# Kernel optimization log

Measured on AMD Instinct MI355X. Metric: run time of the kernel, lower is better.

The kernel has to match this reference:

```python
import jax, jax.numpy as jnp
import numpy as np

SCALE = 2
GROUPS = 4


def setup_inputs() -> dict:
    key = jax.random.key(0)
    k1, k2 = jax.random.split(key)
    x = jax.random.normal(k1, (16, 64, 128, 128), dtype=jnp.float32)
    # offset conv: out_channels = 2*groups*scale^2 = 32, init std=0.001 as in normal_init
    w_off = jax.random.normal(k2, (32, 64), dtype=jnp.float32) * 0.001
    b_off = jnp.zeros((32,), dtype=jnp.float32)
    return {"x": x, "w_off": w_off, "b_off": b_off}


def _init_pos(dtype):
    # h = arange((-s+1)/2, (s-1)/2 + 1) / s ; for s=2 -> [-0.25, 0.25]
    h = (jnp.arange(SCALE, dtype=dtype) - (SCALE - 1) / 2.0) / SCALE
    # channel layout [2, groups, s*s] with p = i*s + j; d=0 -> h[j] (x), d=1 -> h[i] (y)
    hj = jnp.tile(h, SCALE)        # [s*s], value h[p % s]
    hi = jnp.repeat(h, SCALE)      # [s*s], value h[p // s]
    return jnp.stack([hj, hi])[:, None, :]  # [2, 1, s*s] broadcasts over groups


def _grid_sample_border(img, grid):
    # img: [N, C, H, W]; grid: [N, Ho, Wo, 2] in [-1,1], align_corners=False, border padding
    N, C, H, W = img.shape
    gx, gy = grid[..., 0], grid[..., 1]
    ix = jnp.clip(((gx + 1.0) * W - 1.0) * 0.5, 0.0, W - 1.0)
    iy = jnp.clip(((gy + 1.0) * H - 1.0) * 0.5, 0.0, H - 1.0)
    x0f = jnp.floor(ix); y0f = jnp.floor(iy)
    wx = ix - x0f; wy = iy - y0f
    x0 = jnp.clip(x0f.astype(jnp.int32), 0, W - 1)
    x1 = jnp.clip(x0 + 1, 0, W - 1)
    y0 = jnp.clip(y0f.astype(jnp.int32), 0, H - 1)
    y1 = jnp.clip(y0 + 1, 0, H - 1)

    gather = jax.vmap(lambda im, yy, xx: im[:, yy, xx])  # -> [N, C, Ho, Wo]
    v00 = gather(img, y0, x0)
    v01 = gather(img, y0, x1)
    v10 = gather(img, y1, x0)
    v11 = gather(img, y1, x1)
    wx = wx[:, None]; wy = wy[:, None]
    return (1 - wy) * ((1 - wx) * v00 + wx * v01) + wy * ((1 - wx) * v10 + wx * v11)


def reference(x, w_off, b_off):
    B, C, H, W = x.shape
    s, g = SCALE, GROUPS
    # 1x1 offset conv, lp style (no dyscope): offset = conv(x)*0.25 + init_pos
    off = jnp.einsum('bchw,oc->bohw', x, w_off) + b_off[None, :, None, None]
    off = off.reshape(B, 2, g, s * s, H, W) * 0.25 + _init_pos(x.dtype)[None, :, :, :, None, None]
    # pixel centers: x-coord = w+0.5, y-coord = h+0.5
    cx = (jnp.arange(W, dtype=x.dtype) + 0.5)[None, :]  # [1, W]
    cy = (jnp.arange(H, dtype=x.dtype) + 0.5)[:, None]  # [H, 1]
    base = jnp.stack([jnp.broadcast_to(cx, (H, W)), jnp.broadcast_to(cy, (H, W))])  # [2,H,W]
    norm = jnp.array([W, H], dtype=x.dtype).reshape(1, 2, 1, 1, 1, 1)
    coords = 2.0 * (base[None, :, None, None] + off) / norm - 1.0  # [B,2,g,s*s,H,W]
    # pixel_shuffle: output (h*s+i, w*s+j) takes sub-pixel p=i*s+j
    coords = coords.reshape(B, 2, g, s, s, H, W)
    coords = coords.transpose(0, 1, 2, 5, 3, 6, 4).reshape(B, 2, g, s * H, s * W)
    grid = coords.transpose(0, 2, 3, 4, 1).reshape(B * g, s * H, s * W, 2)  # [B*g,sH,sW,2]
    img = x.reshape(B * g, C // g, H, W)
    out = _grid_sample_border(img, grid)
    return out.reshape(B, C, s * H, s * W)
```

## Files before the change

kernel.cpp:

```cpp
#include <hip/hip_runtime.h>


__device__ __forceinline__ float bilerp(float a, float b, float c, float d,
                                        float wx, float wy) {
    const float top = fmaf(wx, b - a, a);
    const float bot = fmaf(wx, d - c, c);
    return fmaf(wy, bot - top, top);
}

__global__ __launch_bounds__(256, 4) void dysample_kernel(
    const float* __restrict__ x, const float* __restrict__ woff,
    const float* __restrict__ boff, float* __restrict__ out)
{
    const int bid = blockIdx.x;
    const int wg  = (bid & 7) * 128 + (bid >> 3);

    const int lane = threadIdx.x & 63;
    const int gr   = __builtin_amdgcn_readfirstlane(threadIdx.x >> 6);
    const int half = lane >> 5;
    const int c    = lane & 31;

    const int b  = wg >> 6;
    const int rp = wg & 63;
    const int h  = 2 * rp + half;

    const float* xb   = x + b * 1048576;
    const float* xrow = xb + h * 128 + 4 * c;

    float acc[8][4];
    #pragma unroll
    for (int j = 0; j < 8; ++j) {
        const float bv = boff[(j < 4) ? (gr * 4 + j) : (12 + gr * 4 + j)];
        #pragma unroll
        for (int p = 0; p < 4; ++p) acc[j][p] = bv;
    }

    #pragma unroll 8
    for (int ch = 0; ch < 64; ++ch) {
        const float4 v = *reinterpret_cast<const float4*>(xrow + ch * 16384);
        #pragma unroll
        for (int j = 0; j < 8; ++j) {
            const int o = (j < 4) ? (gr * 4 + j) : (12 + gr * 4 + j);
            const float wv = woff[o * 64 + ch];
            acc[j][0] = fmaf(v.x, wv, acc[j][0]);
            acc[j][1] = fmaf(v.y, wv, acc[j][1]);
            acc[j][2] = fmaf(v.z, wv, acc[j][2]);
            acc[j][3] = fmaf(v.w, wv, acc[j][3]);
        }
    }

    float wx[4][4], wy[4][4];
    const float fh = (float)h;
    #pragma unroll
    for (int p = 0; p < 4; ++p) {
        const float fwp = (float)(4 * c + p);
        wx[0][p] = fminf(fmaxf(fwp + 0.25f * acc[0][p] - 0.25f, 0.f), 127.f) - (fwp - 1.f);
        wx[1][p] = fminf(fmaxf(fwp + 0.25f * acc[1][p] + 0.25f, 0.f), 127.f) - fwp;
        wx[2][p] = fminf(fmaxf(fwp + 0.25f * acc[2][p] - 0.25f, 0.f), 127.f) - (fwp - 1.f);
        wx[3][p] = fminf(fmaxf(fwp + 0.25f * acc[3][p] + 0.25f, 0.f), 127.f) - fwp;
        wy[0][p] = fminf(fmaxf(fh  + 0.25f * acc[4][p] - 0.25f, 0.f), 127.f) - (fh - 1.f);
        wy[1][p] = fminf(fmaxf(fh  + 0.25f * acc[5][p] - 0.25f, 0.f), 127.f) - (fh - 1.f);
        wy[2][p] = fminf(fmaxf(fh  + 0.25f * acc[6][p] + 0.25f, 0.f), 127.f) - fh;
        wy[3][p] = fminf(fmaxf(fh  + 0.25f * acc[7][p] + 0.25f, 0.f), 127.f) - fh;
    }

    const int hOuter = half ? min(2 * rp + 2, 127) : max(2 * rp - 1, 0);
    const float* gpOuter = xb + gr * 262144 + hOuter * 128 + 4 * c;
    const float* gpMid   = xb + gr * 262144 + h * 128 + 4 * c;

    float* op = out + (size_t)(b * 64 + gr * 16) * 65536
              + (4 * rp + 2 * half) * 256 + 8 * c;

    #pragma unroll 2
    for (int cc = 0; cc < 16; ++cc) {
        const float4 vo = *reinterpret_cast<const float4*>(gpOuter + cc * 16384);
        const float4 vm = *reinterpret_cast<const float4*>(gpMid   + cc * 16384);
        float4 vs;
        vs.x = __shfl_xor(vm.x, 32); vs.y = __shfl_xor(vm.y, 32);
        vs.z = __shfl_xor(vm.z, 32); vs.w = __shfl_xor(vm.w, 32);
        const float4 vt = half ? vs : vo;
        const float4 vb = half ? vo : vs;

        float Lt = __shfl(vt.w, lane - 1); Lt = c ? Lt : vt.x;
        float Lm = __shfl(vm.w, lane - 1); Lm = c ? Lm : vm.x;
        float Lb = __shfl(vb.w, lane - 1); Lb = c ? Lb : vb.x;
        float Rt = __shfl(vt.x, lane + 1); Rt = (c < 31) ? Rt : vt.w;
        float Rm = __shfl(vm.x, lane + 1); Rm = (c < 31) ? Rm : vm.w;
        float Rb = __shfl(vb.x, lane + 1); Rb = (c < 31) ? Rb : vb.w;

        const float tw[6] = {Lt, vt.x, vt.y, vt.z, vt.w, Rt};
        const float mw[6] = {Lm, vm.x, vm.y, vm.z, vm.w, Rm};
        const float bw[6] = {Lb, vb.x, vb.y, vb.z, vb.w, Rb};

        float r0[8], r1[8];
        #pragma unroll
        for (int p = 0; p < 4; ++p) {
            r0[2*p]   = bilerp(tw[p],   tw[p+1], mw[p],   mw[p+1], wx[0][p], wy[0][p]);
            r0[2*p+1] = bilerp(tw[p+1], tw[p+2], mw[p+1], mw[p+2], wx[1][p], wy[1][p]);
            r1[2*p]   = bilerp(mw[p],   mw[p+1], bw[p],   bw[p+1], wx[2][p], wy[2][p]);
            r1[2*p+1] = bilerp(mw[p+1], mw[p+2], bw[p+1], bw[p+2], wx[3][p], wy[3][p]);
        }

        *reinterpret_cast<float4*>(op + 0)   = make_float4(r0[0], r0[1], r0[2], r0[3]);
        *reinterpret_cast<float4*>(op + 4)   = make_float4(r0[4], r0[5], r0[6], r0[7]);
        *reinterpret_cast<float4*>(op + 256) = make_float4(r1[0], r1[1], r1[2], r1[3]);
        *reinterpret_cast<float4*>(op + 260) = make_float4(r1[4], r1[5], r1[6], r1[7]);
        op += 65536;
    }
}

extern "C" void kernel_launch(void* const* d_in, const int* in_sizes, int n_in,
                              void* d_out, int out_size, void* d_ws, size_t ws_size,
                              hipStream_t stream) {
    const float* x    = (const float*)d_in[0];
    const float* woff = (const float*)d_in[1];
    const float* boff = (const float*)d_in[2];
    float* out = (float*)d_out;
    dysample_kernel<<<1024, 256, 0, stream>>>(x, woff, boff, out);
}
```

Before: 78.75 us.

## Remap lanes to two float2 column halves with direct edge loads

Each lane now owns two pairs of columns, 2c..2c+1 and 64+2c..64+2c+1, instead of four consecutive columns. Loads and stores become float2 reads and float4 writes that are contiguous across lanes with smaller per-lane strides. The left and right neighbour pixels are fetched with extra scalar global loads rather than cross-lane shuffles. This is meant to improve coalescing of the output stores and drop the neighbour shuffles. The cost is twelve additional scalar loads per channel, which should mostly hit in cache.

```diff
diff --git a/kernel.cpp b/kernel.cpp
--- a/kernel.cpp
+++ b/kernel.cpp
@@ -25,7 +25,7 @@
     const int h  = 2 * rp + half;
 
     const float* xb   = x + b * 1048576;
-    const float* xrow = xb + h * 128 + 4 * c;
+    const float* xrow = xb + h * 128 + 2 * c;
 
     float acc[8][4];
     #pragma unroll
@@ -37,15 +37,16 @@
 
     #pragma unroll 8
     for (int ch = 0; ch < 64; ++ch) {
-        const float4 v = *reinterpret_cast<const float4*>(xrow + ch * 16384);
+        const float2 va = *reinterpret_cast<const float2*>(xrow + ch * 16384);
+        const float2 vb = *reinterpret_cast<const float2*>(xrow + 64 + ch * 16384);
         #pragma unroll
         for (int j = 0; j < 8; ++j) {
             const int o = (j < 4) ? (gr * 4 + j) : (12 + gr * 4 + j);
             const float wv = woff[o * 64 + ch];
-            acc[j][0] = fmaf(v.x, wv, acc[j][0]);
-            acc[j][1] = fmaf(v.y, wv, acc[j][1]);
-            acc[j][2] = fmaf(v.z, wv, acc[j][2]);
-            acc[j][3] = fmaf(v.w, wv, acc[j][3]);
+            acc[j][0] = fmaf(va.x, wv, acc[j][0]);
+            acc[j][1] = fmaf(va.y, wv, acc[j][1]);
+            acc[j][2] = fmaf(vb.x, wv, acc[j][2]);
+            acc[j][3] = fmaf(vb.y, wv, acc[j][3]);
         }
     }
 
@@ -53,7 +54,7 @@
     const float fh = (float)h;
     #pragma unroll
     for (int p = 0; p < 4; ++p) {
-        const float fwp = (float)(4 * c + p);
+        const float fwp = (float)((p >> 1) * 64 + 2 * c + (p & 1));
         wx[0][p] = fminf(fmaxf(fwp + 0.25f * acc[0][p] - 0.25f, 0.f), 127.f) - (fwp - 1.f);
         wx[1][p] = fminf(fmaxf(fwp + 0.25f * acc[1][p] + 0.25f, 0.f), 127.f) - fwp;
         wx[2][p] = fminf(fmaxf(fwp + 0.25f * acc[2][p] - 0.25f, 0.f), 127.f) - (fwp - 1.f);
@@ -65,46 +66,77 @@
     }
 
     const int hOuter = half ? min(2 * rp + 2, 127) : max(2 * rp - 1, 0);
-    const float* gpOuter = xb + gr * 262144 + hOuter * 128 + 4 * c;
-    const float* gpMid   = xb + gr * 262144 + h * 128 + 4 * c;
+    const int hSib   = 2 * rp + (1 - half);
+    const float* gplane = xb + gr * 262144;
+    const int cAL = max(2 * c - 1, 0);
+    const int cAR = 2 * c + 2;
+    const int cBL = 2 * c + 63;
+    const int cBR = min(2 * c + 66, 127);
+
+    const float* pM  = gplane + h      * 128 + 2 * c;
+    const float* pO  = gplane + hOuter * 128 + 2 * c;
+    const float* pMAL = gplane + h      * 128 + cAL;
+    const float* pMAR = gplane + h      * 128 + cAR;
+    const float* pMBL = gplane + h      * 128 + cBL;
+    const float* pMBR = gplane + h      * 128 + cBR;
+    const float* pOAL = gplane + hOuter * 128 + cAL;
+    const float* pOAR = gplane + hOuter * 128 + cAR;
+    const float* pOBL = gplane + hOuter * 128 + cBL;
+    const float* pOBR = gplane + hOuter * 128 + cBR;
+    const float* pSAL = gplane + hSib   * 128 + cAL;
+    const float* pSAR = gplane + hSib   * 128 + cAR;
+    const float* pSBL = gplane + hSib   * 128 + cBL;
+    const float* pSBR = gplane + hSib   * 128 + cBR;
 
     float* op = out + (size_t)(b * 64 + gr * 16) * 65536
-              + (4 * rp + 2 * half) * 256 + 8 * c;
+              + (4 * rp + 2 * half) * 256 + 4 * c;
 
     #pragma unroll 2
     for (int cc = 0; cc < 16; ++cc) {
-        const float4 vo = *reinterpret_cast<const float4*>(gpOuter + cc * 16384);
-        const float4 vm = *reinterpret_cast<const float4*>(gpMid   + cc * 16384);
-        float4 vs;
-        vs.x = __shfl_xor(vm.x, 32); vs.y = __shfl_xor(vm.y, 32);
-        vs.z = __shfl_xor(vm.z, 32); vs.w = __shfl_xor(vm.w, 32);
-        const float4 vt = half ? vs : vo;
-        const float4 vb = half ? vo : vs;
+        const int co = cc * 16384;
+        const float2 mA = *reinterpret_cast<const float2*>(pM + co);
+        const float2 mB = *reinterpret_cast<const float2*>(pM + 64 + co);
+        const float2 oA = *reinterpret_cast<const float2*>(pO + co);
+        const float2 oB = *reinterpret_cast<const float2*>(pO + 64 + co);
+        const float eMAL = pMAL[co], eMAR = pMAR[co], eMBL = pMBL[co], eMBR = pMBR[co];
+        const float eOAL = pOAL[co], eOAR = pOAR[co], eOBL = pOBL[co], eOBR = pOBR[co];
+        const float eSAL = pSAL[co], eSAR = pSAR[co], eSBL = pSBL[co], eSBR = pSBR[co];
 
-        float Lt = __shfl(vt.w, lane - 1); Lt = c ? Lt : vt.x;
-        float Lm = __shfl(vm.w, lane - 1); Lm = c ? Lm : vm.x;
-        float Lb = __shfl(vb.w, lane - 1); Lb = c ? Lb : vb.x;
-        float Rt = __shfl(vt.x, lane + 1); Rt = (c < 31) ? Rt : vt.w;
-        float Rm = __shfl(vm.x, lane + 1); Rm = (c < 31) ? Rm : vm.w;
-        float Rb = __shfl(vb.x, lane + 1); Rb = (c < 31) ? Rb : vb.w;
+        float2 sA, sB;
+        sA.x = __shfl_xor(mA.x, 32); sA.y = __shfl_xor(mA.y, 32);
+        sB.x = __shfl_xor(mB.x, 32); sB.y = __shfl_xor(mB.y, 32);
 
-        const float tw[6] = {Lt, vt.x, vt.y, vt.z, vt.w, Rt};
-        const float mw[6] = {Lm, vm.x, vm.y, vm.z, vm.w, Rm};
-        const float bw[6] = {Lb, vb.x, vb.y, vb.z, vb.w, Rb};
+        const float2 tA = half ? sA : oA, bA = half ? oA : sA;
+        const float2 tB = half ? sB : oB, bB = half ? oB : sB;
+        const float eTAL = half ? eSAL : eOAL, eTAR = half ? eSAR : eOAR;
+        const float eTBL = half ? eSBL : eOBL, eTBR = half ? eSBR : eOBR;
+        const float eBAL = half ? eOAL : eSAL, eBAR = half ? eOAR : eSAR;
+        const float eBBL = half ? eOBL : eSBL, eBBR = half ? eOBR : eSBR;
 
-        float r0[8], r1[8];
+        const float twA[4] = {eTAL, tA.x, tA.y, eTAR};
+        const float mwA[4] = {eMAL, mA.x, mA.y, eMAR};
+        const float bwA[4] = {eBAL, bA.x, bA.y, eBAR};
+        const float twB[4] = {eTBL, tB.x, tB.y, eTBR};
+        const float mwB[4] = {eMBL, mB.x, mB.y, eMBR};
+        const float bwB[4] = {eBBL, bB.x, bB.y, eBBR};
+
+        float rtA[4], rbA[4], rtB[4], rbB[4];
         #pragma unroll
-        for (int p = 0; p < 4; ++p) {
-            r0[2*p]   = bilerp(tw[p],   tw[p+1], mw[p],   mw[p+1], wx[0][p], wy[0][p]);
-            r0[2*p+1] = bilerp(tw[p+1], tw[p+2], mw[p+1], mw[p+2], wx[1][p], wy[1][p]);
-            r1[2*p]   = bilerp(mw[p],   mw[p+1], bw[p],   bw[p+1], wx[2][p], wy[2][p]);
-            r1[2*p+1] = bilerp(mw[p+1], mw[p+2], bw[p+1], bw[p+2], wx[3][p], wy[3][p]);
+        for (int p = 0; p < 2; ++p) {
+            rtA[2*p]   = bilerp(twA[p],   twA[p+1], mwA[p],   mwA[p+1], wx[0][p], wy[0][p]);
+            rtA[2*p+1] = bilerp(twA[p+1], twA[p+2], mwA[p+1], mwA[p+2], wx[1][p], wy[1][p]);
+            rbA[2*p]   = bilerp(mwA[p],   mwA[p+1], bwA[p],   bwA[p+1], wx[2][p], wy[2][p]);
+            rbA[2*p+1] = bilerp(mwA[p+1], mwA[p+2], bwA[p+1], bwA[p+2], wx[3][p], wy[3][p]);
+            rtB[2*p]   = bilerp(twB[p],   twB[p+1], mwB[p],   mwB[p+1], wx[0][p+2], wy[0][p+2]);
+            rtB[2*p+1] = bilerp(twB[p+1], twB[p+2], mwB[p+1], mwB[p+2], wx[1][p+2], wy[1][p+2]);
+            rbB[2*p]   = bilerp(mwB[p],   mwB[p+1], bwB[p],   bwB[p+1], wx[2][p+2], wy[2][p+2]);
+            rbB[2*p+1] = bilerp(mwB[p+1], mwB[p+2], bwB[p+1], bwB[p+2], wx[3][p+2], wy[3][p+2]);
         }
 
-        *reinterpret_cast<float4*>(op + 0)   = make_float4(r0[0], r0[1], r0[2], r0[3]);
-        *reinterpret_cast<float4*>(op + 4)   = make_float4(r0[4], r0[5], r0[6], r0[7]);
-        *reinterpret_cast<float4*>(op + 256) = make_float4(r1[0], r1[1], r1[2], r1[3]);
-        *reinterpret_cast<float4*>(op + 260) = make_float4(r1[4], r1[5], r1[6], r1[7]);
+        *reinterpret_cast<float4*>(op + 0)         = make_float4(rtA[0], rtA[1], rtA[2], rtA[3]);
+        *reinterpret_cast<float4*>(op + 128)       = make_float4(rtB[0], rtB[1], rtB[2], rtB[3]);
+        *reinterpret_cast<float4*>(op + 256)       = make_float4(rbA[0], rbA[1], rbA[2], rbA[3]);
+        *reinterpret_cast<float4*>(op + 256 + 128) = make_float4(rbB[0], rbB[1], rbB[2], rbB[3]);
         op += 65536;
     }
 }
```

After: 80.29 us. No clear change (+2.0%).
